# Kernel tuning notes

Measured on AMD Instinct MI355X. Metric: run time of the kernel, lower is better.

Reference implementation:

```python
import math
import jax, jax.numpy as jnp
import numpy as np
from jax.scipy.special import xlogy, gammaln

DIM = 768
HEADS = 8
DIM_KEY = 64
DIM_VALUE = 64
NUM_REL_POS_FEATURES = 192
B = 2
N = 2048


def get_positional_embed(seq_len, feature_size):
    # distances: [-n+1, ..., n-1], length 2n-1
    dist = jnp.arange(-seq_len + 1, seq_len).astype(jnp.float32)
    ad = jnp.abs(dist)[:, None]  # [2n-1, 1]
    nb = feature_size // 6  # num basis per class (3 fns, doubled by sign concat)

    # exponential
    max_range = math.log(seq_len) / math.log(2.0)
    half_life = 2.0 ** jnp.linspace(3.0, max_range, nb)  # min_half_life = 3.0
    f_exp = jnp.exp(-math.log(2.0) / half_life[None, :] * ad)

    # central mask
    widths = 2.0 ** jnp.arange(1, nb + 1).astype(jnp.float32) - 1.0
    f_cm = (widths[None, :] > ad).astype(jnp.float32)

    # gamma pdf
    stddev = seq_len / (2.0 * nb)
    start_mean = seq_len / nb
    mean = jnp.linspace(start_mean, float(seq_len), nb)[None, :]
    conc = (mean / stddev) ** 2
    rate = mean / (stddev ** 2)
    log_unnorm = xlogy(conc - 1.0, ad) - rate * ad
    log_norm = gammaln(conc) - conc * jnp.log(rate)
    prob = jnp.exp(log_unnorm - log_norm) + 1e-8
    f_g = prob / jnp.max(prob, axis=-1, keepdims=True)

    emb = jnp.concatenate([f_exp, f_cm, f_g], axis=-1)  # [2n-1, 3*nb]
    emb = jnp.concatenate([emb, jnp.sign(dist)[:, None] * emb], axis=-1)  # [2n-1, 6*nb]
    return emb


def relative_shift(x):
    # x: [b, h, t1, 2*t1 - 1] -> [b, h, t1, t1] via pad/reshape trick
    b, h, t1, t2 = x.shape
    x = jnp.pad(x, ((0, 0), (0, 0), (0, 0), (1, 0)))  # [b,h,t1,t2+1]
    x = x.reshape(b, h, t2 + 1, t1)[:, :, 1:, :].reshape(b, h, t1, t2)
    return x[..., : (t2 + 2) // 2]


def setup_inputs() -> dict:
    key = jax.random.key(0)
    ks = jax.random.split(key, 9)
    dk, dv, h = DIM_KEY, DIM_VALUE, HEADS
    s_in = 1.0 / math.sqrt(DIM)
    s_rel = 1.0 / math.sqrt(NUM_REL_POS_FEATURES)
    s_out = 1.0 / math.sqrt(dv * h)
    return {
        "x": jax.random.normal(ks[0], (B, N, DIM), dtype=jnp.float32),
        # weights stored [in, out] (torch Linear weight transposed)
        "Wq": jax.random.normal(ks[1], (DIM, dk * h), dtype=jnp.float32) * s_in,
        "Wk": jax.random.normal(ks[2], (DIM, dk * h), dtype=jnp.float32) * s_in,
        "Wv": jax.random.normal(ks[3], (DIM, dv * h), dtype=jnp.float32) * s_in,
        "Wrel": jax.random.normal(ks[4], (NUM_REL_POS_FEATURES, dk * h), dtype=jnp.float32) * s_rel,
        # module inits to_out at zeros; use random values for a meaningful baseline
        "Wout": jax.random.normal(ks[5], (dv * h, DIM), dtype=jnp.float32) * s_out,
        "b_out": jax.random.normal(ks[6], (DIM,), dtype=jnp.float32) * 0.01,
        "rel_content_bias": jax.random.normal(ks[7], (1, h, 1, dk), dtype=jnp.float32),
        "rel_pos_bias": jax.random.normal(ks[8], (1, h, 1, dk), dtype=jnp.float32),
    }


def reference(x, Wq, Wk, Wv, Wrel, Wout, b_out, rel_content_bias, rel_pos_bias):
    b, n, _ = x.shape
    h, dk = HEADS, DIM_KEY
    scale = dk ** -0.5

    q = (x @ Wq).reshape(b, n, h, dk).transpose(0, 2, 1, 3) * scale  # [b,h,n,dk]
    k = (x @ Wk).reshape(b, n, h, dk).transpose(0, 2, 1, 3)
    v = (x @ Wv).reshape(b, n, h, -1).transpose(0, 2, 1, 3)  # [b,h,n,dv]

    content_logits = jnp.einsum('bhid,bhjd->bhij', q + rel_content_bias, k)

    positions = get_positional_embed(n, NUM_REL_POS_FEATURES)  # [2n-1, F]
    rel_k = (positions @ Wrel).reshape(2 * n - 1, h, dk).transpose(1, 0, 2)  # [h,2n-1,dk]
    rel_logits = jnp.einsum('bhid,hjd->bhij', q + rel_pos_bias, rel_k)  # [b,h,n,2n-1]
    rel_logits = relative_shift(rel_logits)  # [b,h,n,n]

    attn = jax.nn.softmax(content_logits + rel_logits, axis=-1)
    out = jnp.einsum('bhij,bhjd->bhid', attn, v)  # [b,h,n,dv]
    out = out.transpose(0, 2, 1, 3).reshape(b, n, -1)  # [b,n,h*dv]
    return out @ Wout + b_out
```

## Files before the change

kernel.cpp:

```cpp
#include <hip/hip_runtime.h>
#include <hip/hip_bf16.h>
#include <math.h>
#include <stdint.h>

typedef __hip_bfloat16 bf16;
typedef __attribute__((ext_vector_type(8))) short short8;
typedef __attribute__((ext_vector_type(4))) float f32x4;

#define SEQ   2048
#define NPOS  4095
#define DIMM  768
#define HEADS 8
#define DK    64
#define HD    512
#define BATCH 2
#define BH    16
#define ROWS  4096

#define OB_RELK  ((size_t)0)
#define OB_QC    ((size_t)4194304)
#define OB_QP    ((size_t)8388608)
#define OB_K     ((size_t)12582912)
#define OB_V     ((size_t)16777216)
#define OB_OH    ((size_t)20971520)
#define OB_EMBH  OB_OH
#define OB_EMBL  ((size_t)(OB_OH + 1572864))
#define OB_XH    ((size_t)25165824)
#define OB_XL    ((size_t)31457280)
#define OB_WQKVH ((size_t)37748736)
#define OB_WQKVL ((size_t)40108032)
#define OB_OP    ((size_t)25165824)
#define OB_LP    ((size_t)41943040)
#define OB_WOH   ((size_t)42467328)
#define OB_WOL   ((size_t)43253760)
#define OB_WRH   ((size_t)44040192)
#define OB_WRL   ((size_t)44236800)

__device__ __forceinline__ unsigned f2bf(float f) {
  unsigned u = __float_as_uint(f);
  return (u + 0x7fffu + ((u >> 16) & 1u)) >> 16;
}
__device__ __forceinline__ void split2(float v, unsigned& hb, unsigned& lb) {
  hb = f2bf(v);
  const float back = __uint_as_float(hb << 16);
  lb = f2bf(v - back);
}

__device__ __forceinline__ void cp16(const short* g, short* l) {
  __builtin_amdgcn_global_load_lds(
      (__attribute__((address_space(1))) void*)(uintptr_t)(g),
      (__attribute__((address_space(3))) void*)(uint32_t)(uintptr_t)(l),
      16, 0, 0);
}

__global__ __launch_bounds__(256) void prep_all(
    const float* __restrict__ x,
    const float* __restrict__ Wq, const float* __restrict__ Wk,
    const float* __restrict__ Wv, const float* __restrict__ Wout,
    const float* __restrict__ Wrel,
    short* __restrict__ eh, short* __restrict__ el,
    short* __restrict__ xh, short* __restrict__ xl,
    short* __restrict__ wqkvh, short* __restrict__ wqkvl,
    short* __restrict__ woh, short* __restrict__ wol,
    short* __restrict__ wrh, short* __restrict__ wrl) {
  __shared__ float tile[32][33];
  const int blk = blockIdx.x;
  const int t = threadIdx.x;

  if (blk < 512) {
    const int row = blk * 8 + (t >> 5);
    const int j   = t & 31;
    if (row >= NPOS) {
      for (int c = j; c < 192; c += 32) { eh[(size_t)row * 192 + c] = 0; el[(size_t)row * 192 + c] = 0; }
      return;
    }
    const float dist = (float)(row - (SEQ - 1));
    const float ad   = fabsf(dist);
    const float hl    = exp2f(3.0f + 8.0f * (float)j / 31.0f);
    const float f_exp = exp2f(-ad / hl);
    const float width = exp2f((float)(j + 1)) - 1.0f;
    const float f_cm  = (width > ad) ? 1.0f : 0.0f;
    float prob;
    if (ad > 0.0f) {
      const float c   = 4.0f * (float)((j + 1) * (j + 1));
      const float r   = (float)(j + 1) / 16.0f;
      const float lu  = (c - 1.0f) * logf(ad) - r * ad;
      const float ln_ = lgammaf(c) - c * logf(r);
      prob = expf(lu - ln_) + 1e-8f;
    } else {
      prob = 1e-8f;
    }
    float mx = prob;
    for (int off = 16; off; off >>= 1) mx = fmaxf(mx, __shfl_xor(mx, off, 32));
    const float f_g = prob / mx;
    const float s = (dist > 0.f) ? 1.f : ((dist < 0.f) ? -1.f : 0.f);
    const float vals[6] = {f_exp, f_cm, f_g, s * f_exp, s * f_cm, s * f_g};
    short* ph = eh + (size_t)row * 192;
    short* pl = el + (size_t)row * 192;
#pragma unroll
    for (int q = 0; q < 6; q++) {
      unsigned hb, lb;
      split2(vals[q], hb, lb);
      ph[q * 32 + j] = (short)hb;
      pl[q * 32 + j] = (short)lb;
    }
    return;
  }

  if (blk < 3584) {
    const int i = (blk - 512) * 256 + t;
    const float4 v = ((const float4*)x)[i];
    unsigned h0, l0, h1, l1, h2, l2, h3, l3;
    split2(v.x, h0, l0); split2(v.y, h1, l1); split2(v.z, h2, l2); split2(v.w, h3, l3);
    *(uint2*)&xh[(size_t)i * 4] = make_uint2(h0 | (h1 << 16), h2 | (h3 << 16));
    *(uint2*)&xl[(size_t)i * 4] = make_uint2(l0 | (l1 << 16), l2 | (l3 << 16));
    return;
  }

  const float* src; short* dh; short* dl; int R, C, local;
  if (blk < 3968)      { local = blk - 3584; src = Wq;   dh = wqkvh;               dl = wqkvl;               R = DIMM; C = HD; }
  else if (blk < 4352) { local = blk - 3968; src = Wk;   dh = wqkvh + 512 * DIMM;  dl = wqkvl + 512 * DIMM;  R = DIMM; C = HD; }
  else if (blk < 4736) { local = blk - 4352; src = Wv;   dh = wqkvh + 1024 * DIMM; dl = wqkvl + 1024 * DIMM; R = DIMM; C = HD; }
  else if (blk < 5120) { local = blk - 4736; src = Wout; dh = woh;  dl = wol;  R = HD;  C = DIMM; }
  else                 { local = blk - 5120; src = Wrel; dh = wrh;  dl = wrl;  R = 192; C = HD; }
  const int ctiles = C / 32;
  const int c0 = (local % ctiles) * 32, r0 = (local / ctiles) * 32;
  {
    const int lr = t >> 3, lc = (t & 7) * 4;
    const float4 v = *(const float4*)&src[(size_t)(r0 + lr) * C + c0 + lc];
    tile[lr][lc] = v.x; tile[lr][lc + 1] = v.y; tile[lr][lc + 2] = v.z; tile[lr][lc + 3] = v.w;
  }
  __syncthreads();
  const int nn = t >> 3, kb = (t & 7) * 4;
  unsigned hb[4], lb[4];
#pragma unroll
  for (int e = 0; e < 4; e++) split2(tile[kb + e][nn], hb[e], lb[e]);
  const size_t o = (size_t)(c0 + nn) * R + r0 + kb;
  *(uint2*)&dh[o] = make_uint2(hb[0] | (hb[1] << 16), hb[2] | (hb[3] << 16));
  *(uint2*)&dl[o] = make_uint2(lb[0] | (lb[1] << 16), lb[2] | (lb[3] << 16));
}

__global__ __launch_bounds__(256) void gemm_qr(
    const short* __restrict__ xh, const short* __restrict__ xl,
    const short* __restrict__ wqkvh, const short* __restrict__ wqkvl,
    const short* __restrict__ eh, const short* __restrict__ el,
    const short* __restrict__ wrh, const short* __restrict__ wrl,
    const float* __restrict__ cb, const float* __restrict__ pb,
    bf16* __restrict__ oq, bf16* __restrict__ oqp,
    bf16* __restrict__ ok, short* __restrict__ vtw,
    bf16* __restrict__ relk) {
  __shared__ short AsH[128][32];
  __shared__ short AsL[128][32];
  __shared__ short BsH[128][32];
  __shared__ short BsL[128][32];

  const int bx = blockIdx.x;
  const bool isq = bx < 384;
  const int lbx = isq ? bx : bx - 384;
  const int mt = lbx & 31, ntile = lbx >> 5;
  const int m0 = mt * 128, n0 = ntile * 128;
  const int KD = isq ? DIMM : 192;
  const short* Ah = isq ? xh : eh;
  const short* Al = isq ? xl : el;
  const short* Bh = isq ? wqkvh : wrh;
  const short* Bl = isq ? wqkvl : wrl;

  const int t = threadIdx.x, lane = t & 63, w = t >> 6;
  const int quad = lane >> 4, l15 = lane & 15;
  const int wm = (w >> 1) * 64, wn = (w & 1) * 64;

  const int srow = w * 32 + (lane >> 2);
  const int skof = (lane & 3) * 8;

  f32x4 acc[4][4];
#pragma unroll
  for (int i = 0; i < 4; i++)
#pragma unroll
    for (int j = 0; j < 4; j++) acc[i][j] = (f32x4){0.f, 0.f, 0.f, 0.f};

  for (int k0 = 0; k0 < KD; k0 += 32) {
    __syncthreads();
#pragma unroll
    for (int c = 0; c < 2; c++) {
      const size_t ra = (size_t)(m0 + srow + c * 16) * KD + k0 + skof;
      const size_t rb = (size_t)(n0 + srow + c * 16) * KD + k0 + skof;
      cp16(&Ah[ra], &AsH[w * 32 + c * 16][0]);
      cp16(&Al[ra], &AsL[w * 32 + c * 16][0]);
      cp16(&Bh[rb], &BsH[w * 32 + c * 16][0]);
      cp16(&Bl[rb], &BsL[w * 32 + c * 16][0]);
    }
    __syncthreads();

    short8 amh[4], aml[4], bnh[4], bnl[4];
#pragma unroll
    for (int i = 0; i < 4; i++) {
      amh[i] = *(const short8*)&AsH[wm + i * 16 + l15][quad * 8];
      aml[i] = *(const short8*)&AsL[wm + i * 16 + l15][quad * 8];
      bnh[i] = *(const short8*)&BsH[wn + i * 16 + l15][quad * 8];
      bnl[i] = *(const short8*)&BsL[wn + i * 16 + l15][quad * 8];
    }
#pragma unroll
    for (int i = 0; i < 4; i++) {
#pragma unroll
      for (int j = 0; j < 4; j++) {
        acc[i][j] = __builtin_amdgcn_mfma_f32_16x16x32_bf16(amh[i], bnh[j], acc[i][j], 0, 0, 0);
        acc[i][j] = __builtin_amdgcn_mfma_f32_16x16x32_bf16(amh[i], bnl[j], acc[i][j], 0, 0, 0);
        acc[i][j] = __builtin_amdgcn_mfma_f32_16x16x32_bf16(aml[i], bnh[j], acc[i][j], 0, 0, 0);
      }
    }
  }

  if (isq) {
    const int sel = ntile >> 2;
    if (sel == 2) {
#pragma unroll
      for (int i = 0; i < 4; i++) {
#pragma unroll
        for (int j = 0; j < 4; j++) {
          const int n = n0 + wn + j * 16 + l15;
          const int hd_ = n & 511, hh = hd_ >> 6, d = hd_ & 63;
          const int m = m0 + wm + i * 16 + quad * 4;
          const int b = m >> 11, s = m & 2047;
          const uint2 pk = make_uint2(
              f2bf(acc[i][j][0]) | (f2bf(acc[i][j][1]) << 16),
              f2bf(acc[i][j][2]) | (f2bf(acc[i][j][3]) << 16));
          *(uint2*)&vtw[(((size_t)(b * HEADS + hh) * DK + d) * SEQ) + s] = pk;
        }
      }
    } else {
#pragma unroll
      for (int i = 0; i < 4; i++) {
#pragma unroll
        for (int j = 0; j < 4; j++) {
          const int n = n0 + wn + j * 16 + l15;
          const int hd_ = n & 511, hh = hd_ >> 6, d = hd_ & 63;
#pragma unroll
          for (int g = 0; g < 4; g++) {
            const int m = m0 + wm + i * 16 + quad * 4 + g;
            const int b = m >> 11, s = m & 2047;
            const size_t idx = (((size_t)(b * HEADS + hh) * SEQ) + s) * DK + d;
            const float v = acc[i][j][g];
            if (sel == 0) {
              const float sv = v * 0.125f;
              oq[idx]  = __float2bfloat16(sv + cb[hh * DK + d]);
              oqp[idx] = __float2bfloat16(sv + pb[hh * DK + d]);
            } else {
              ok[idx] = __float2bfloat16(v);
            }
          }
        }
      }
    }
  } else {
#pragma unroll
    for (int i = 0; i < 4; i++) {
#pragma unroll
      for (int j = 0; j < 4; j++) {
        const int n = n0 + wn + j * 16 + l15;
        const int hh = n >> 6, d = n & 63;
#pragma unroll
        for (int g = 0; g < 4; g++) {
          const int m = m0 + wm + i * 16 + quad * 4 + g;
          if (m < NPOS) relk[((size_t)hh * NPOS + m) * DK + d] = __float2bfloat16(acc[i][j][g]);
        }
      }
    }
  }
}

__global__ __launch_bounds__(256) void out_gemm(
    const short* __restrict__ Ahp,
    const short* __restrict__ Bhp, const short* __restrict__ Blp,
    const float* __restrict__ bias, float* __restrict__ ofp) {
  __shared__ short AsH[128][32];
  __shared__ short BsH[128][32];
  __shared__ short BsL[128][32];

  const int t = threadIdx.x, lane = t & 63, w = t >> 6;
  const int quad = lane >> 4, l15 = lane & 15;
  const int wm = (w >> 1) * 64, wn = (w & 1) * 64;
  const int m0 = blockIdx.x * 128, n0 = blockIdx.y * 128;
  const int srow = w * 32 + (lane >> 2);
  const int skof = (lane & 3) * 8;

  f32x4 acc[4][4];
#pragma unroll
  for (int i = 0; i < 4; i++)
#pragma unroll
    for (int j = 0; j < 4; j++) acc[i][j] = (f32x4){0.f, 0.f, 0.f, 0.f};

  for (int k0 = 0; k0 < HD; k0 += 32) {
    __syncthreads();
#pragma unroll
    for (int c = 0; c < 2; c++) {
      const size_t ra = (size_t)(m0 + srow + c * 16) * HD + k0 + skof;
      const size_t rb = (size_t)(n0 + srow + c * 16) * HD + k0 + skof;
      cp16(&Ahp[ra], &AsH[w * 32 + c * 16][0]);
      cp16(&Bhp[rb], &BsH[w * 32 + c * 16][0]);
      cp16(&Blp[rb], &BsL[w * 32 + c * 16][0]);
    }
    __syncthreads();

    short8 amh[4], bnh[4], bnl[4];
#pragma unroll
    for (int i = 0; i < 4; i++) {
      amh[i] = *(const short8*)&AsH[wm + i * 16 + l15][quad * 8];
      bnh[i] = *(const short8*)&BsH[wn + i * 16 + l15][quad * 8];
      bnl[i] = *(const short8*)&BsL[wn + i * 16 + l15][quad * 8];
    }
#pragma unroll
    for (int i = 0; i < 4; i++) {
#pragma unroll
      for (int j = 0; j < 4; j++) {
        acc[i][j] = __builtin_amdgcn_mfma_f32_16x16x32_bf16(amh[i], bnh[j], acc[i][j], 0, 0, 0);
        acc[i][j] = __builtin_amdgcn_mfma_f32_16x16x32_bf16(amh[i], bnl[j], acc[i][j], 0, 0, 0);
      }
    }
  }

#pragma unroll
  for (int i = 0; i < 4; i++) {
#pragma unroll
    for (int j = 0; j < 4; j++) {
      const int n = n0 + wn + j * 16 + l15;
      const float bv = bias[n];
#pragma unroll
      for (int g = 0; g < 4; g++) {
        const int m = m0 + wm + i * 16 + quad * 4 + g;
        ofp[(size_t)m * DIMM + n] = acc[i][j][g] + bv;
      }
    }
  }
}

__global__ __launch_bounds__(256) void attn_mfma4(
    const short* __restrict__ qc, const short* __restrict__ qp,
    const short* __restrict__ kg, const short* __restrict__ vt,
    const short* __restrict__ relk,
    float* __restrict__ Op, float* __restrict__ Lp) {
  __shared__ short Rel_lds[128][72];
  __shared__ short Vt_lds[64][72];
  __shared__ short Pw[4][16][72];

  const int bid = blockIdx.x;
  const int swz = (bid & 7) * 128 + (bid >> 3);
  const int i0  = (swz & 31) * 64;
  const int bh  = (swz >> 5) & 15;
  const int z   = swz >> 9;
  const int h   = bh & 7;
  const int jb  = z * (SEQ / 2);

  const int t    = threadIdx.x;
  const int lane = t & 63;
  const int w    = t >> 6;
  const int quad = lane >> 4;
  const int l15  = lane & 15;

  short8 qcA[2], qpA[2];
  {
    const size_t qrow = ((size_t)bh * SEQ + i0 + w * 16 + l15) * DK + quad * 8;
    qcA[0] = *(const short8*)(qc + qrow);
    qcA[1] = *(const short8*)(qc + qrow + 32);
    qpA[0] = *(const short8*)(qp + qrow);
    qpA[1] = *(const short8*)(qp + qrow + 32);
  }

  int idxg[4]; bool selg[4];
#pragma unroll
  for (int g = 0; g < 4; g++) {
    const int r = quad * 4 + g;
    idxg[g] = (((lane & 48) | ((l15 + 15 - r) & 15)) << 2);
    selg[g] = (l15 <= r);
  }

  short8 ones8;
#pragma unroll
  for (int e = 0; e < 8; e++) ones8[e] = (short)0x3F80;

  f32x4 oacc[4];
#pragma unroll
  for (int dt = 0; dt < 4; dt++) oacc[dt] = (f32x4){0.f, 0.f, 0.f, 0.f};
  f32x4 lacc = (f32x4){0.f, 0.f, 0.f, 0.f};

  const short* kbase = kg + (size_t)bh * SEQ * DK;
  const short* vbase = vt + (size_t)bh * DK * SEQ;
  const short* rbase = relk + ((size_t)(h * NPOS + 1984 - i0)) * DK;

  const int rr  = 16 + (t >> 1), rcc = (t & 1) * 32;
  const int vr  = t >> 2, vcc = (t & 3) * 16;
  const int rb_w = 48 - 16 * w;

  f32x4 bpp_carry;
  {
    const short* rl = rbase + (size_t)(jb + rb_w + l15) * DK + quad * 8;
    short8 b0 = *(const short8*)rl;
    short8 b1 = *(const short8*)(rl + 32);
    f32x4 a = (f32x4){0.f, 0.f, 0.f, 0.f};
    a = __builtin_amdgcn_mfma_f32_16x16x32_bf16(qpA[0], b0, a, 0, 0, 0);
    a = __builtin_amdgcn_mfma_f32_16x16x32_bf16(qpA[1], b1, a, 0, 0, 0);
#pragma unroll
    for (int g = 0; g < 4; g++)
      bpp_carry[g] = __int_as_float(__builtin_amdgcn_ds_bpermute(idxg[g], __float_as_int(a[g])));
  }

  for (int jt = 0; jt < SEQ / 2 / 64; jt++) {
    const int j0 = jb + jt * 64;

    __syncthreads();
    if (rr < 128) {
      const short* src = rbase + (size_t)(j0 + rr) * DK + rcc;
      *(uint4*)&Rel_lds[rr][rcc]      = *(const uint4*)(src);
      *(uint4*)&Rel_lds[rr][rcc + 8]  = *(const uint4*)(src + 8);
      *(uint4*)&Rel_lds[rr][rcc + 16] = *(const uint4*)(src + 16);
      *(uint4*)&Rel_lds[rr][rcc + 24] = *(const uint4*)(src + 24);
    }
    {
      const short* src = vbase + (size_t)vr * SEQ + j0 + vcc;
      *(uint4*)&Vt_lds[vr][vcc]     = *(const uint4*)(src);
      *(uint4*)&Vt_lds[vr][vcc + 8] = *(const uint4*)(src + 8);
    }
    __syncthreads();

    f32x4 sacc[4];
#pragma unroll
    for (int nt = 0; nt < 4; nt++) {
      const short* kr = kbase + (size_t)(j0 + nt * 16 + l15) * DK + quad * 8;
      short8 b0 = *(const short8*)kr;
      short8 b1 = *(const short8*)(kr + 32);
      f32x4 a = (f32x4){0.f, 0.f, 0.f, 0.f};
      a = __builtin_amdgcn_mfma_f32_16x16x32_bf16(qcA[0], b0, a, 0, 0, 0);
      a = __builtin_amdgcn_mfma_f32_16x16x32_bf16(qcA[1], b1, a, 0, 0, 0);
      sacc[nt] = a;
    }

    f32x4 bpp = bpp_carry;

#pragma unroll
    for (int nt = 0; nt < 4; nt++) {
      f32x4 rcur;
      {
        const short* rl = &Rel_lds[rb_w + (nt + 1) * 16 + l15][quad * 8];
        short8 b0 = *(const short8*)rl;
        short8 b1 = *(const short8*)(rl + 32);
        f32x4 a = (f32x4){0.f, 0.f, 0.f, 0.f};
        a = __builtin_amdgcn_mfma_f32_16x16x32_bf16(qpA[0], b0, a, 0, 0, 0);
        a = __builtin_amdgcn_mfma_f32_16x16x32_bf16(qpA[1], b1, a, 0, 0, 0);
        rcur = a;
      }
      f32x4 bpc;
#pragma unroll
      for (int g = 0; g < 4; g++)
        bpc[g] = __int_as_float(__builtin_amdgcn_ds_bpermute(idxg[g], __float_as_int(rcur[g])));
#pragma unroll
      for (int g = 0; g < 4; g++) {
        const float relv = selg[g] ? bpp[g] : bpc[g];
        const float s = sacc[nt][g] + relv;
        const float p = __expf(s - 12.0f);
        Pw[w][quad * 4 + g][nt * 16 + l15] = (short)f2bf(p);
      }
      bpp = bpc;
    }
    bpp_carry = bpp;

#pragma unroll
    for (int ks = 0; ks < 2; ks++) {
      short8 pA = *(const short8*)&Pw[w][l15][ks * 32 + quad * 8];
      lacc = __builtin_amdgcn_mfma_f32_16x16x32_bf16(pA, ones8, lacc, 0, 0, 0);
#pragma unroll
      for (int dt = 0; dt < 4; dt++) {
        short8 vB = *(const short8*)&Vt_lds[dt * 16 + l15][ks * 32 + quad * 8];
        oacc[dt] = __builtin_amdgcn_mfma_f32_16x16x32_bf16(pA, vB, oacc[dt], 0, 0, 0);
      }
    }
  }

  const size_t obase = ((size_t)(z * BH + bh) * SEQ + i0 + w * 16);
#pragma unroll
  for (int g = 0; g < 4; g++) {
    const int r = quad * 4 + g;
#pragma unroll
    for (int dt = 0; dt < 4; dt++)
      Op[(obase + r) * DK + dt * 16 + l15] = oacc[dt][g];
    if (l15 == 0) Lp[obase + r] = lacc[g];
  }
}

__global__ void merge_kernel(const float* __restrict__ Op, const float* __restrict__ Lp,
                             bf16* __restrict__ oh) {
  const int gid = blockIdx.x * 256 + threadIdx.x;
  const int m = gid >> 7;
  const int n0 = (gid & 127) * 4;
  const int b = m >> 11, s = m & 2047;
  const int hh = n0 >> 6, d0 = n0 & 63;
  const int bh = b * HEADS + hh;
  const float l = Lp[(size_t)bh * SEQ + s] + Lp[((size_t)BH + bh) * SEQ + s];
  const float inv = 1.0f / l;
  const float4 o0 = *(const float4*)&Op[((size_t)bh * SEQ + s) * DK + d0];
  const float4 o1 = *(const float4*)&Op[(((size_t)BH + bh) * SEQ + s) * DK + d0];
  *(uint2*)&oh[(size_t)m * HD + n0] = make_uint2(
      f2bf((o0.x + o1.x) * inv) | (f2bf((o0.y + o1.y) * inv) << 16),
      f2bf((o0.z + o1.z) * inv) | (f2bf((o0.w + o1.w) * inv) << 16));
}

extern "C" void kernel_launch(void* const* d_in, const int* in_sizes, int n_in,
                              void* d_out, int out_size, void* d_ws, size_t ws_size,
                              hipStream_t stream) {
  (void)in_sizes; (void)n_in; (void)out_size; (void)ws_size;
  const float* x    = (const float*)d_in[0];
  const float* Wq   = (const float*)d_in[1];
  const float* Wk   = (const float*)d_in[2];
  const float* Wv   = (const float*)d_in[3];
  const float* Wrel = (const float*)d_in[4];
  const float* Wout = (const float*)d_in[5];
  const float* bout = (const float*)d_in[6];
  const float* cb   = (const float*)d_in[7];
  const float* pb   = (const float*)d_in[8];
  float* out = (float*)d_out;

  char* ws = (char*)d_ws;
  bf16*  relk = (bf16*)(ws + OB_RELK);
  bf16*  qc   = (bf16*)(ws + OB_QC);
  bf16*  qp   = (bf16*)(ws + OB_QP);
  bf16*  kk   = (bf16*)(ws + OB_K);
  short* vt   = (short*)(ws + OB_V);
  bf16*  oh   = (bf16*)(ws + OB_OH);
  float* Opb  = (float*)(ws + OB_OP);
  float* Lpb  = (float*)(ws + OB_LP);
  short* embh = (short*)(ws + OB_EMBH);
  short* embl = (short*)(ws + OB_EMBL);
  short* xh   = (short*)(ws + OB_XH);
  short* xl   = (short*)(ws + OB_XL);
  short* wqh  = (short*)(ws + OB_WQKVH);
  short* wql  = (short*)(ws + OB_WQKVL);
  short* woh  = (short*)(ws + OB_WOH);
  short* wol  = (short*)(ws + OB_WOL);
  short* wrh  = (short*)(ws + OB_WRH);
  short* wrl  = (short*)(ws + OB_WRL);

  hipLaunchKernelGGL(prep_all, dim3(5216), dim3(256), 0, stream,
                     x, Wq, Wk, Wv, Wout, Wrel,
                     embh, embl, xh, xl, wqh, wql, woh, wol, wrh, wrl);
  hipLaunchKernelGGL(gemm_qr, dim3(512), dim3(256), 0, stream,
                     xh, xl, wqh, wql, embh, embl, wrh, wrl,
                     cb, pb, qc, qp, kk, vt, relk);
  hipLaunchKernelGGL(attn_mfma4, dim3(1024), dim3(256), 0, stream,
                     (const short*)qc, (const short*)qp, (const short*)kk,
                     (const short*)vt, (const short*)relk, Opb, Lpb);
  hipLaunchKernelGGL(merge_kernel, dim3(ROWS * (HD / 4) / 256), dim3(256), 0, stream,
                     Opb, Lpb, oh);
  hipLaunchKernelGGL(out_gemm, dim3(32, 6), dim3(256), 0, stream,
                     (const short*)oh, woh, wol, bout, out);
}
```

Baseline: 236.3 us.

## Double-buffer attention LDS tiles with async copies and XOR-swizzled layouts

The attention kernel now stages the relative-key and V^T tiles into two alternating LDS buffers with 16-byte async copies (cp16). The next tile is prefetched while the current one is being computed, so there is one barrier per iteration instead of two. The projection GEMM writes relk and vt in an XOR-swizzled column order, which lets the unpadded LDS tiles be read without bank conflicts and copied straight from global memory. The cost is double the LDS staging footprint and a global layout that only this kernel's indexing understands.

```diff
diff --git a/kernel.cpp b/kernel.cpp
--- a/kernel.cpp
+++ b/kernel.cpp
@@ -221,10 +221,11 @@
           const int hd_ = n & 511, hh = hd_ >> 6, d = hd_ & 63;
           const int m = m0 + wm + i * 16 + quad * 4;
           const int b = m >> 11, s = m & 2047;
+          const int s_swz = s ^ ((d & 7) << 3);
           const uint2 pk = make_uint2(
               f2bf(acc[i][j][0]) | (f2bf(acc[i][j][1]) << 16),
               f2bf(acc[i][j][2]) | (f2bf(acc[i][j][3]) << 16));
-          *(uint2*)&vtw[(((size_t)(b * HEADS + hh) * DK + d) * SEQ) + s] = pk;
+          *(uint2*)&vtw[(((size_t)(b * HEADS + hh) * DK + d) * SEQ) + s_swz] = pk;
         }
       }
     } else {
@@ -261,7 +262,9 @@
 #pragma unroll
         for (int g = 0; g < 4; g++) {
           const int m = m0 + wm + i * 16 + quad * 4 + g;
-          if (m < NPOS) relk[((size_t)hh * NPOS + m) * DK + d] = __float2bfloat16(acc[i][j][g]);
+          if (m < NPOS)
+            relk[((size_t)hh * NPOS + m) * DK + (d ^ ((m & 7) << 3))] =
+                __float2bfloat16(acc[i][j][g]);
         }
       }
     }
@@ -338,8 +341,8 @@
     const short* __restrict__ kg, const short* __restrict__ vt,
     const short* __restrict__ relk,
     float* __restrict__ Op, float* __restrict__ Lp) {
-  __shared__ short Rel_lds[128][72];
-  __shared__ short Vt_lds[64][72];
+  __shared__ __align__(16) short RelB[2][112 * 64];
+  __shared__ __align__(16) short VtB[2][64 * 64];
   __shared__ short Pw[4][16][72];
 
   const int bid = blockIdx.x;
@@ -355,6 +358,7 @@
   const int w    = t >> 6;
   const int quad = lane >> 4;
   const int l15  = lane & 15;
+  const int x    = (l15 & 7) << 3;
 
   short8 qcA[2], qpA[2];
   {
@@ -386,15 +390,29 @@
   const short* vbase = vt + (size_t)bh * DK * SEQ;
   const short* rbase = relk + ((size_t)(h * NPOS + 1984 - i0)) * DK;
 
-  const int rr  = 16 + (t >> 1), rcc = (t & 1) * 32;
-  const int vr  = t >> 2, vcc = (t & 3) * 16;
   const int rb_w = 48 - 16 * w;
 
+  auto STAGE = [&](int nxt, int j0n) {
+    const short* rsrc = rbase + (size_t)(j0n + 16) * DK;
+#pragma unroll
+    for (int cc = 0; cc < 6; cc++) {
+      const int c = w + cc * 4;
+      if (c < 14) {
+        cp16(rsrc + c * 512 + lane * 8, &RelB[nxt][c * 512]);
+      } else if (c < 22) {
+        const int cv = c - 14;
+        cp16(vbase + (size_t)(cv * 8 + (lane >> 3)) * SEQ + j0n + (lane & 7) * 8,
+             &VtB[nxt][cv * 512]);
+      }
+    }
+  };
+
+  STAGE(0, jb);
   f32x4 bpp_carry;
   {
-    const short* rl = rbase + (size_t)(jb + rb_w + l15) * DK + quad * 8;
-    short8 b0 = *(const short8*)rl;
-    short8 b1 = *(const short8*)(rl + 32);
+    const short* rl = rbase + (size_t)(jb + rb_w + l15) * DK;
+    short8 b0 = *(const short8*)(rl + ((quad * 8) ^ x));
+    short8 b1 = *(const short8*)(rl + ((quad * 8 + 32) ^ x));
     f32x4 a = (f32x4){0.f, 0.f, 0.f, 0.f};
     a = __builtin_amdgcn_mfma_f32_16x16x32_bf16(qpA[0], b0, a, 0, 0, 0);
     a = __builtin_amdgcn_mfma_f32_16x16x32_bf16(qpA[1], b1, a, 0, 0, 0);
@@ -402,24 +420,13 @@
     for (int g = 0; g < 4; g++)
       bpp_carry[g] = __int_as_float(__builtin_amdgcn_ds_bpermute(idxg[g], __float_as_int(a[g])));
   }
-
-  for (int jt = 0; jt < SEQ / 2 / 64; jt++) {
+  __syncthreads();
+
+  int cur = 0;
+  for (int jt = 0; jt < 16; jt++) {
     const int j0 = jb + jt * 64;
 
-    __syncthreads();
-    if (rr < 128) {
-      const short* src = rbase + (size_t)(j0 + rr) * DK + rcc;
-      *(uint4*)&Rel_lds[rr][rcc]      = *(const uint4*)(src);
-      *(uint4*)&Rel_lds[rr][rcc + 8]  = *(const uint4*)(src + 8);
-      *(uint4*)&Rel_lds[rr][rcc + 16] = *(const uint4*)(src + 16);
-      *(uint4*)&Rel_lds[rr][rcc + 24] = *(const uint4*)(src + 24);
-    }
-    {
-      const short* src = vbase + (size_t)vr * SEQ + j0 + vcc;
-      *(uint4*)&Vt_lds[vr][vcc]     = *(const uint4*)(src);
-      *(uint4*)&Vt_lds[vr][vcc + 8] = *(const uint4*)(src + 8);
-    }
-    __syncthreads();
+    if (jt < 15) STAGE(cur ^ 1, j0 + 64);
 
     f32x4 sacc[4];
 #pragma unroll
@@ -439,9 +446,9 @@
     for (int nt = 0; nt < 4; nt++) {
       f32x4 rcur;
       {
-        const short* rl = &Rel_lds[rb_w + (nt + 1) * 16 + l15][quad * 8];
-        short8 b0 = *(const short8*)rl;
-        short8 b1 = *(const short8*)(rl + 32);
+        const short* rl = &RelB[cur][(rb_w + nt * 16 + l15) * 64];
+        short8 b0 = *(const short8*)(rl + ((quad * 8) ^ x));
+        short8 b1 = *(const short8*)(rl + ((quad * 8 + 32) ^ x));
         f32x4 a = (f32x4){0.f, 0.f, 0.f, 0.f};
         a = __builtin_amdgcn_mfma_f32_16x16x32_bf16(qpA[0], b0, a, 0, 0, 0);
         a = __builtin_amdgcn_mfma_f32_16x16x32_bf16(qpA[1], b1, a, 0, 0, 0);
@@ -468,10 +475,14 @@
       lacc = __builtin_amdgcn_mfma_f32_16x16x32_bf16(pA, ones8, lacc, 0, 0, 0);
 #pragma unroll
       for (int dt = 0; dt < 4; dt++) {
-        short8 vB = *(const short8*)&Vt_lds[dt * 16 + l15][ks * 32 + quad * 8];
+        const short* vl = &VtB[cur][(dt * 16 + l15) * 64 + (((ks * 32 + quad * 8)) ^ x)];
+        short8 vB = *(const short8*)vl;
         oacc[dt] = __builtin_amdgcn_mfma_f32_16x16x32_bf16(pA, vB, oacc[dt], 0, 0, 0);
       }
     }
+
+    __syncthreads();
+    cur ^= 1;
   }
 
   const size_t obase = ((size_t)(z * BH + bh) * SEQ + i0 + w * 16);
```

Result: slower. 251.9 us (+6.6%).
